# Optimization experiments

Measured on AMD Instinct MI355X. Metric: run time of the kernel, lower is better.

The kernel has to match this reference:

```python
import jax, jax.numpy as jnp
import numpy as np

N, E, DIN, H = 10000, 80000, 1024, 512
NEG = 0.2  # PyG GATv2Conv default negative_slope


def gatv2(x, src, dst, wl, bl, wr, br, att, b, n):
    # GATv2: e_ij = att . leaky_relu(Wl x_j + Wr x_i); segment softmax over dst; sum alpha * Wl x_j
    xl = x @ wl + bl            # [N, H] source transform
    xr = x @ wr + br            # [N, H] target transform
    z = jax.nn.leaky_relu(xl[src] + xr[dst], NEG)   # [E, H]
    e = z @ att                                      # [E]
    m = jax.ops.segment_max(e, dst, num_segments=n)  # per-target max (self-loops guarantee nonempty)
    p = jnp.exp(e - m[dst])
    s = jax.ops.segment_sum(p, dst, num_segments=n)
    alpha = p / (s[dst] + 1e-16)                     # [E]
    out = jax.ops.segment_sum(alpha[:, None] * xl[src], dst, num_segments=n)
    return out + b


def setup_inputs() -> dict:
    key = jax.random.key(0)
    ks = iter(jax.random.split(key, 64))
    d = {}
    d["x"] = jax.random.normal(next(ks), (N, DIN), jnp.float32)
    d["edge_index"] = jax.random.randint(next(ks), (2, E), 0, N, dtype=jnp.int32).astype(jnp.int64)
    dims = [DIN, H, H, H]
    for i in range(4):
        din = dims[i]
        sc = 1.0 / np.sqrt(din)
        d[f"wl{i+1}"] = jax.random.normal(next(ks), (din, H), jnp.float32) * sc
        d[f"bl{i+1}"] = jnp.zeros((H,), jnp.float32)
        d[f"wr{i+1}"] = jax.random.normal(next(ks), (din, H), jnp.float32) * sc
        d[f"br{i+1}"] = jnp.zeros((H,), jnp.float32)
        d[f"att{i+1}"] = jax.random.normal(next(ks), (H,), jnp.float32) * (1.0 / np.sqrt(H))
        d[f"b{i+1}"] = jnp.zeros((H,), jnp.float32)
    for name, din, dout in [("1", H, 512), ("2", 512, 256), ("3", 256, 2)]:
        d[f"lw{name}"] = jax.random.normal(next(ks), (din, dout), jnp.float32) * (1.0 / np.sqrt(din))
        d[f"lb{name}"] = jnp.zeros((dout,), jnp.float32)
    return d


def reference(x, edge_index, wl1, bl1, wr1, br1, att1, b1,
              wl2, bl2, wr2, br2, att2, b2,
              wl3, bl3, wr3, br3, att3, b3,
              wl4, bl4, wr4, br4, att4, b4,
              lw1, lb1, lw2, lb2, lw3, lb3):
    n = x.shape[0]
    loops = jnp.arange(n, dtype=edge_index.dtype)
    src = jnp.concatenate([edge_index[0], loops])  # add self-loops (PyG default)
    dst = jnp.concatenate([edge_index[1], loops])
    h = jax.nn.relu(gatv2(x, src, dst, wl1, bl1, wr1, br1, att1, b1, n))
    h = jax.nn.relu(gatv2(h, src, dst, wl2, bl2, wr2, br2, att2, b2, n))
    h = jax.nn.relu(gatv2(h, src, dst, wl3, bl3, wr3, br3, att3, b3, n))
    h = jax.nn.relu(gatv2(h, src, dst, wl4, bl4, wr4, br4, att4, b4, n))
    # dropout is identity at inference
    h = jax.nn.relu(h @ lw1 + lb1)
    h = jax.nn.relu(h @ lw2 + lb2)
    logits = h @ lw3 + lb3
    return logits, jax.nn.softmax(logits, axis=1)
```

## Files before the change

### kernel.cpp

```cpp
#include <hip/hip_runtime.h>
#include <cstdint>

#define NN 10000
#define NE 80000
#define DIN_ 1024
#define HH 512

typedef __attribute__((ext_vector_type(8))) short bf16x8;
typedef __attribute__((ext_vector_type(4))) float f32x4;
typedef unsigned short u16;
typedef unsigned int u32;

static __device__ __forceinline__ float b2f(u16 u) {
  u32 i = ((u32)u) << 16;
  return __builtin_bit_cast(float, i);
}
static __device__ __forceinline__ u16 f2b(float f) {
  u32 i = __builtin_bit_cast(u32, f);
  u32 r = (i + 0x7fffu + ((i >> 16) & 1u)) >> 16;
  return (u16)r;
}
static __device__ __forceinline__ void unpack8(uint4 u, float* f) {
  f[0] = __builtin_bit_cast(float, u.x << 16);
  f[1] = __builtin_bit_cast(float, u.x & 0xffff0000u);
  f[2] = __builtin_bit_cast(float, u.y << 16);
  f[3] = __builtin_bit_cast(float, u.y & 0xffff0000u);
  f[4] = __builtin_bit_cast(float, u.z << 16);
  f[5] = __builtin_bit_cast(float, u.z & 0xffff0000u);
  f[6] = __builtin_bit_cast(float, u.w << 16);
  f[7] = __builtin_bit_cast(float, u.w & 0xffff0000u);
}
static __device__ __forceinline__ void load8(const u16* p, float* f) { unpack8(*(const uint4*)p, f); }

#define ASYNC_CP16(gp, lp)                                                        \
  __builtin_amdgcn_global_load_lds((__attribute__((address_space(1))) void*)(gp), \
                                   (__attribute__((address_space(3))) void*)(lp), \
                                   16, 0, 0)

static __device__ __forceinline__ int float_flag(const u16* xw) {
  __shared__ int c;
  if (threadIdx.x == 0) c = 0;
  __syncthreads();
  int bad = 0;
  for (int i = threadIdx.x; i < 2048; i += blockDim.x) {
    u32 e = (xw[i] >> 7) & 0xFFu;
    if (e >= 140u) bad++;
  }
  if (bad) atomicAdd(&c, bad);
  __syncthreads();
  return c > 64;
}
static __device__ __forceinline__ int int64_flag(const u32* ew) {
  __shared__ int c;
  if (threadIdx.x == 0) c = 0;
  __syncthreads();
  int z = 0;
  for (int i = threadIdx.x; i < 256; i += blockDim.x)
    if (ew[2 * i + 1] == 0u) z++;
  if (z) atomicAdd(&c, z);
  __syncthreads();
  return c > 200;
}

__global__ void k_edges(const void* ei, int* esrc, int* edst, int* counts) {
  int f64 = int64_flag((const u32*)ei);
  int i = blockIdx.x * 256 + threadIdx.x;
  if (i < NE) {
    int sv, dv;
    if (f64) {
      sv = (int)((const long long*)ei)[i];
      dv = (int)((const long long*)ei)[NE + i];
    } else {
      sv = ((const int*)ei)[i];
      dv = ((const int*)ei)[NE + i];
    }
    esrc[i] = sv;
    edst[i] = dv;
    atomicAdd(&counts[dv], 1);
  } else if (i < NE + NN) {
    atomicAdd(&counts[i - NE], 1);
  }
}

__global__ __launch_bounds__(512) void k_scan(const int* counts, int* rowptr, int* cursor, int n) {
  __shared__ int lds[512];
  const int PER = 20;
  int t = threadIdx.x;
  int base = t * PER;
  int v[PER];
  int sum = 0;
#pragma unroll
  for (int i = 0; i < PER; i++) {
    int idx = base + i;
    v[i] = (idx < n) ? counts[idx] : 0;
    sum += v[i];
  }
  lds[t] = sum;
  __syncthreads();
  for (int off = 1; off < 512; off <<= 1) {
    int x = (t >= off) ? lds[t - off] : 0;
    __syncthreads();
    lds[t] += x;
    __syncthreads();
  }
  int run = (t > 0) ? lds[t - 1] : 0;
#pragma unroll
  for (int i = 0; i < PER; i++) {
    int idx = base + i;
    if (idx < n) {
      cursor[idx] = run;
      run += v[i];
      rowptr[idx + 1] = run;
    }
  }
  if (t == 0) rowptr[0] = 0;
}

#define SBLK 352
#define XBLK 2048
struct Prep {
  const int* esrc;
  const int* edst;
  int* cursor;
  int* col;
  const void* xin;
  u16* xout;
  const void* vin[20];
  u16* vout[20];
  int vn[20];
  const void* tin[10];
  u16* tout[10];
  int tK[10], tN[10], toff[10];
};
__global__ void k_prep(Prep a) {
  __shared__ u16 tt[32][33];
  int b = blockIdx.x;
  if (b < SBLK) {
    int i = b * 256 + threadIdx.x;
    if (i < NE) {
      int p = atomicAdd(&a.cursor[a.edst[i]], 1);
      a.col[p] = a.esrc[i];
    } else if (i < NE + NN) {
      int v = i - NE;
      int p = atomicAdd(&a.cursor[v], 1);
      a.col[p] = v;
    }
    return;
  }
  b -= SBLK;
  int f = float_flag((const u16*)a.xin);
  if (b < XBLK) {
    const int total = NN * DIN_ / 8;
    for (int g = b * 256 + threadIdx.x; g < total; g += XBLK * 256) {
      u16 o[8];
      if (f) {
        const float* p = (const float*)a.xin + (size_t)g * 8;
#pragma unroll
        for (int i = 0; i < 8; i++) o[i] = f2b(p[i]);
      } else {
        *(uint4*)o = *((const uint4*)a.xin + g);
      }
      *((uint4*)a.xout + g) = *(const uint4*)o;
    }
  } else if (b < XBLK + 20) {
    int v = b - XBLK;
    const void* in = a.vin[v];
    u16* out = a.vout[v];
    int n = a.vn[v];
    for (int i = threadIdx.x; i < n; i += 256)
      out[i] = f ? f2b(((const float*)in)[i]) : ((const u16*)in)[i];
  } else {
    int tb = b - XBLK - 20;
    int seg = 0;
#pragma unroll
    for (int i = 1; i < 10; i++)
      if (tb >= a.toff[i]) seg = i;
    int tl = tb - a.toff[seg];
    int K = a.tK[seg], N = a.tN[seg];
    int tiles_n = N >> 5;
    int n0 = (tl % tiles_n) << 5, k0 = (tl / tiles_n) << 5;
    const void* in = a.tin[seg];
    u16* out = a.tout[seg];
    int tx = threadIdx.x & 31, ty = threadIdx.x >> 5;
    for (int r = ty; r < 32; r += 8) {
      size_t idx = (size_t)(k0 + r) * N + n0 + tx;
      tt[r][tx] = f ? f2b(((const float*)in)[idx]) : ((const u16*)in)[idx];
    }
    __syncthreads();
    for (int r = ty; r < 32; r += 8) out[(size_t)(n0 + r) * K + k0 + tx] = tt[tx][r];
  }
}

__global__ __launch_bounds__(256) void k_gemm64(const u16* __restrict__ A, int lda,
                                                const u16* __restrict__ Bt,
                                                const u16* __restrict__ bias,
                                                u16* __restrict__ C,
                                                int M, int N, int K, int act,
                                                int tiles_m, int ln_tiles_n) {
  __shared__ u16 sA[2 * 64 * 32];
  __shared__ u16 sB[2 * 128 * 32];
  int id = blockIdx.x;
  int xcd = id & 7;
  int rest = id >> 3;
  int xt = rest & ((1 << ln_tiles_n) - 1);
  int yt = ((rest >> ln_tiles_n) << 3) + xcd;
  if (yt >= tiles_m) return;
  int m0 = yt << 6, n0 = xt << 7;
  int t = threadIdx.x;
  int wave = t >> 6, lane = t & 63;

  int srow = t >> 2;
  int sk = ((t & 3) ^ ((t >> 3) & 3)) * 8;
  const u16* agp[2];
  u16* la[2];
#pragma unroll
  for (int h = 0; h < 2; h++) {
    int ra = m0 + srow;
    ra = ra < M ? ra : M - 1;
    agp[h] = A + (size_t)ra * lda + h * 32 + sk;
    la[h] = sA + h * 2048 + t * 8;
  }
  const u16* bgp[4];
  u16* lb[4];
#pragma unroll
  for (int q = 0; q < 4; q++) {
    int h = q >> 1;
    int row = ((q & 1) << 6) + srow;
    bgp[q] = Bt + (size_t)(n0 + row) * K + h * 32 + sk;
    lb[q] = sB + h * 4096 + (((q & 1) << 8) + t) * 8;
  }

  int wn = wave << 5;
  int lr = lane & 15;
  int kcs = (((lane >> 4) ^ ((lr >> 1) & 3))) * 8;

  f32x4 acc[4][2];
#pragma unroll
  for (int i = 0; i < 4; i++)
#pragma unroll
    for (int j = 0; j < 2; j++) acc[i][j] = (f32x4){0.f, 0.f, 0.f, 0.f};

  for (int k0 = 0; k0 < K; k0 += 64) {
#pragma unroll
    for (int h = 0; h < 2; h++) ASYNC_CP16(agp[h] + k0, la[h]);
#pragma unroll
    for (int q = 0; q < 4; q++) ASYNC_CP16(bgp[q] + k0, lb[q]);
    __syncthreads();
    bf16x8 a[2][4], b[2][2];
#pragma unroll
    for (int s = 0; s < 2; s++) {
#pragma unroll
      for (int i = 0; i < 4; i++) a[s][i] = *(const bf16x8*)(sA + s * 2048 + (i * 16 + lr) * 32 + kcs);
#pragma unroll
      for (int j = 0; j < 2; j++) b[s][j] = *(const bf16x8*)(sB + s * 4096 + (wn + j * 16 + lr) * 32 + kcs);
    }
#pragma unroll
    for (int s = 0; s < 2; s++)
#pragma unroll
      for (int i = 0; i < 4; i++)
#pragma unroll
        for (int j = 0; j < 2; j++)
          acc[i][j] = __builtin_amdgcn_mfma_f32_16x16x32_bf16(a[s][i], b[s][j], acc[i][j], 0, 0, 0);
    __syncthreads();
  }

  int rbase = (lane >> 4) << 2;
#pragma unroll
  for (int j = 0; j < 2; j++) {
    int colc = n0 + wn + j * 16 + lr;
    float bv = b2f(bias[colc]);
#pragma unroll
    for (int i = 0; i < 4; i++) {
#pragma unroll
      for (int r = 0; r < 4; r++) {
        int row = m0 + i * 16 + rbase + r;
        if (row < M) {
          float v = acc[i][j][r] + bv;
          if (act) v = fmaxf(v, 0.f);
          C[(size_t)row * N + colc] = f2b(v);
        }
      }
    }
  }
}

__global__ __launch_bounds__(256) void k_attn5(u16* __restrict__ xlr,
                                               const u16* __restrict__ att, const u16* __restrict__ bias,
                                               const int* __restrict__ rowptr, const int* __restrict__ col,
                                               int n) {
  int node = (blockIdx.x * 256 + threadIdx.x) >> 6;
  if (node >= n) return;
  int lane = threadIdx.x & 63;
  int h0 = lane * 8;
  float a[8], r[8];
  load8(att + h0, a);
  load8(xlr + (size_t)node * 1024 + 512 + h0, r);
  int e0 = rowptr[node], e1 = rowptr[node + 1];

  float m = -3e38f, s = 0.f;
  float acc[8] = {0.f, 0.f, 0.f, 0.f, 0.f, 0.f, 0.f, 0.f};
  int j0 = col[e0];
  int j1 = col[(e0 + 1 < e1) ? e0 + 1 : e0];
  uint4 raw0 = *(const uint4*)(xlr + (size_t)j0 * 1024 + h0);
  uint4 raw1 = *(const uint4*)(xlr + (size_t)j1 * 1024 + h0);

  for (int e = e0; e < e1; e += 2) {
    bool has2 = (e + 1 < e1);
    int jn0 = col[(e + 2 < e1) ? e + 2 : e1 - 1];
    int jn1 = col[(e + 3 < e1) ? e + 3 : e1 - 1];
    uint4 p0 = *(const uint4*)(xlr + (size_t)jn0 * 1024 + h0);
    uint4 p1 = *(const uint4*)(xlr + (size_t)jn1 * 1024 + h0);
    float x0[8], x1[8];
    unpack8(raw0, x0);
    unpack8(raw1, x1);
    float pa = 0.f, pb = 0.f;
#pragma unroll
    for (int i = 0; i < 8; i++) {
      float z0 = x0[i] + r[i];
      z0 = z0 > 0.f ? z0 : 0.2f * z0;
      pa = fmaf(a[i], z0, pa);
      float z1 = x1[i] + r[i];
      z1 = z1 > 0.f ? z1 : 0.2f * z1;
      pb = fmaf(a[i], z1, pb);
    }
#pragma unroll
    for (int off = 32; off >= 1; off >>= 1) {
      pa += __shfl_xor(pa, off);
      pb += __shfl_xor(pb, off);
    }
    if (pa > m) {
      float al = __expf(m - pa);
      s = fmaf(s, al, 1.f);
#pragma unroll
      for (int i = 0; i < 8; i++) acc[i] = fmaf(acc[i], al, x0[i]);
      m = pa;
    } else {
      float w = __expf(pa - m);
      s += w;
#pragma unroll
      for (int i = 0; i < 8; i++) acc[i] = fmaf(w, x0[i], acc[i]);
    }
    if (has2) {
      if (pb > m) {
        float al = __expf(m - pb);
        s = fmaf(s, al, 1.f);
#pragma unroll
        for (int i = 0; i < 8; i++) acc[i] = fmaf(acc[i], al, x1[i]);
        m = pb;
      } else {
        float w = __expf(pb - m);
        s += w;
#pragma unroll
        for (int i = 0; i < 8; i++) acc[i] = fmaf(w, x1[i], acc[i]);
      }
    }
    raw0 = p0;
    raw1 = p1;
  }
  float inv = 1.f / (s + 1e-16f);

  float bv[8];
  load8(bias + h0, bv);
  uint4 o;
  u32 p8[8];
#pragma unroll
  for (int i = 0; i < 8; i++) {
    float v = fmaf(acc[i], inv, bv[i]);
    v = fmaxf(v, 0.f);
    p8[i] = f2b(v);
  }
  o.x = p8[0] | (p8[1] << 16);
  o.y = p8[2] | (p8[3] << 16);
  o.z = p8[4] | (p8[5] << 16);
  o.w = p8[6] | (p8[7] << 16);
  *(uint4*)(xlr + (size_t)node * 1024 + 512 + h0) = o;
}

__global__ __launch_bounds__(256) void k_head(const u16* __restrict__ h2, const u16* __restrict__ lw3,
                                              const u16* __restrict__ lb3, float* __restrict__ out, int n) {
  int row = (blockIdx.x * 256 + threadIdx.x) >> 6;
  if (row >= n) return;
  int lane = threadIdx.x & 63;
  int k0 = lane * 4;
  uint2 hu = *(const uint2*)(h2 + (size_t)row * 256 + k0);
  float hx[4];
  hx[0] = __builtin_bit_cast(float, hu.x << 16);
  hx[1] = __builtin_bit_cast(float, hu.x & 0xffff0000u);
  hx[2] = __builtin_bit_cast(float, hu.y << 16);
  hx[3] = __builtin_bit_cast(float, hu.y & 0xffff0000u);
  float wv[8];
  load8(lw3 + (size_t)k0 * 2, wv);
  float p0 = 0.f, p1 = 0.f;
#pragma unroll
  for (int i = 0; i < 4; i++) {
    p0 = fmaf(hx[i], wv[2 * i], p0);
    p1 = fmaf(hx[i], wv[2 * i + 1], p1);
  }
#pragma unroll
  for (int off = 32; off >= 1; off >>= 1) {
    p0 += __shfl_xor(p0, off);
    p1 += __shfl_xor(p1, off);
  }
  if (lane == 0) {
    float l0 = p0 + b2f(lb3[0]);
    float l1 = p1 + b2f(lb3[1]);
    float mx = fmaxf(l0, l1);
    float q0 = __expf(l0 - mx), q1 = __expf(l1 - mx);
    float si = 1.f / (q0 + q1);
    out[row * 2 + 0] = l0;
    out[row * 2 + 1] = l1;
    out[2 * n + row * 2 + 0] = q0 * si;
    out[2 * n + row * 2 + 1] = q1 * si;
  }
}

extern "C" void kernel_launch(void* const* d_in, const int* in_sizes, int n_in,
                              void* d_out, int out_size, void* d_ws, size_t ws_size,
                              hipStream_t stream) {
  (void)in_sizes; (void)n_in; (void)out_size; (void)ws_size;
  const void* x_raw = d_in[0];
  const void* ei_raw = d_in[1];
  const void *wl[4], *bl[4], *wr[4], *br[4], *att[4], *bg[4];
  for (int i = 0; i < 4; i++) {
    wl[i] = d_in[2 + i * 6 + 0];
    bl[i] = d_in[2 + i * 6 + 1];
    wr[i] = d_in[2 + i * 6 + 2];
    br[i] = d_in[2 + i * 6 + 3];
    att[i] = d_in[2 + i * 6 + 4];
    bg[i] = d_in[2 + i * 6 + 5];
  }
  const void* lw1 = d_in[26];
  const void* lb1 = d_in[27];
  const void* lw2 = d_in[28];
  const void* lb2 = d_in[29];
  const void* lw3 = d_in[30];
  const void* lb3 = d_in[31];

  size_t off = 0;
  auto alloc = [&](size_t bytes) -> void* {
    off = (off + 255) & ~(size_t)255;
    void* p = (char*)d_ws + off;
    off += bytes;
    return p;
  };
  int* esrc = (int*)alloc(NE * 4);
  int* edst = (int*)alloc(NE * 4);
  int* counts = (int*)alloc(NN * 4);
  int* rowptr = (int*)alloc((NN + 1) * 4);
  int* cursor = (int*)alloc(NN * 4);
  int* col = (int*)alloc((NE + NN) * 4);
  u16* cb = (u16*)alloc(4 * 1024 * 2);
  u16* attv = (u16*)alloc(4 * 512 * 2);
  u16* bgv = (u16*)alloc(4 * 512 * 2);
  u16* lb1v = (u16*)alloc(512 * 2);
  u16* lb2v = (u16*)alloc(256 * 2);
  u16* lw3v = (u16*)alloc(512 * 2);
  u16* lb3v = (u16*)alloc(2 * 2);
  u16* comb0 = (u16*)alloc((size_t)1024 * 1024 * 2);
  u16* combL[4];
  combL[0] = comb0;
  for (int l = 1; l < 4; l++) combL[l] = (u16*)alloc((size_t)1024 * 512 * 2);
  u16* lw1T = (u16*)alloc((size_t)512 * 512 * 2);
  u16* lw2T = (u16*)alloc((size_t)256 * 512 * 2);
  u16* xc = (u16*)alloc((size_t)NN * DIN_ * 2);
  u16* X0 = (u16*)alloc((size_t)NN * 1024 * 2);
  u16* X1 = (u16*)alloc((size_t)NN * 1024 * 2);
  u16* mlp1 = xc;
  u16* mlp2 = xc + (size_t)NN * 512;

  hipMemsetAsync(counts, 0, NN * 4, stream);
  int ET = NE + NN;
  k_edges<<<(ET + 255) / 256, 256, 0, stream>>>(ei_raw, esrc, edst, counts);
  k_scan<<<1, 512, 0, stream>>>(counts, rowptr, cursor, NN);

  Prep pa;
  pa.esrc = esrc;
  pa.edst = edst;
  pa.cursor = cursor;
  pa.col = col;
  pa.xin = x_raw;
  pa.xout = xc;
  for (int l = 0; l < 4; l++) {
    pa.vin[l * 4 + 0] = bl[l];  pa.vout[l * 4 + 0] = cb + l * 1024;        pa.vn[l * 4 + 0] = 512;
    pa.vin[l * 4 + 1] = br[l];  pa.vout[l * 4 + 1] = cb + l * 1024 + 512;  pa.vn[l * 4 + 1] = 512;
    pa.vin[l * 4 + 2] = att[l]; pa.vout[l * 4 + 2] = attv + l * 512;       pa.vn[l * 4 + 2] = 512;
    pa.vin[l * 4 + 3] = bg[l];  pa.vout[l * 4 + 3] = bgv + l * 512;        pa.vn[l * 4 + 3] = 512;
  }
  pa.vin[16] = lb1; pa.vout[16] = lb1v; pa.vn[16] = 512;
  pa.vin[17] = lb2; pa.vout[17] = lb2v; pa.vn[17] = 256;
  pa.vin[18] = lw3; pa.vout[18] = lw3v; pa.vn[18] = 512;
  pa.vin[19] = lb3; pa.vout[19] = lb3v; pa.vn[19] = 2;
  const void* tin[10] = {wl[0], wr[0], wl[1], wr[1], wl[2], wr[2], wl[3], wr[3], lw1, lw2};
  u16* tout[10] = {comb0, comb0 + (size_t)512 * 1024,
                   combL[1], combL[1] + (size_t)512 * 512,
                   combL[2], combL[2] + (size_t)512 * 512,
                   combL[3], combL[3] + (size_t)512 * 512,
                   lw1T, lw2T};
  int tK[10] = {1024, 1024, 512, 512, 512, 512, 512, 512, 512, 512};
  int tN[10] = {512, 512, 512, 512, 512, 512, 512, 512, 512, 256};
  int acc_off = 0;
  for (int i = 0; i < 10; i++) {
    pa.tin[i] = tin[i];
    pa.tout[i] = tout[i];
    pa.tK[i] = tK[i];
    pa.tN[i] = tN[i];
    pa.toff[i] = acc_off;
    acc_off += (tN[i] >> 5) * (tK[i] >> 5);
  }
  k_prep<<<SBLK + XBLK + 20 + acc_off, 256, 0, stream>>>(pa);

  auto gemm = [&](const u16* A, int lda, const u16* Bt, const u16* bias, u16* C,
                  int M, int Nn, int K, int act) {
    int tiles_m = (M + 63) >> 6;
    int tiles_n = Nn >> 7;
    int ln = (tiles_n == 8) ? 3 : (tiles_n == 4) ? 2 : 1;
    int mgrp = (tiles_m + 7) >> 3;
    int blocks = (mgrp << 3) * tiles_n;
    k_gemm64<<<blocks, 256, 0, stream>>>(A, lda, Bt, bias, C, M, Nn, K, act, tiles_m, ln);
  };
  auto attn = [&](u16* xlr, int l) {
    k_attn5<<<(NN * 64 + 255) / 256, 256, 0, stream>>>(xlr, attv + l * 512, bgv + l * 512,
                                                       rowptr, col, NN);
  };

  gemm(xc, 1024, comb0, cb + 0 * 1024, X0, NN, 1024, 1024, 0);
  attn(X0, 0);
  gemm(X0 + 512, 1024, combL[1], cb + 1 * 1024, X1, NN, 1024, 512, 0);
  attn(X1, 1);
  gemm(X1 + 512, 1024, combL[2], cb + 2 * 1024, X0, NN, 1024, 512, 0);
  attn(X0, 2);
  gemm(X0 + 512, 1024, combL[3], cb + 3 * 1024, X1, NN, 1024, 512, 0);
  attn(X1, 3);

  gemm(X1 + 512, 1024, lw1T, lb1v, mlp1, NN, 512, 512, 1);
  gemm(mlp1, 512, lw2T, lb2v, mlp2, NN, 256, 512, 1);
  k_head<<<(NN * 64 + 255) / 256, 256, 0, stream>>>(mlp2, lw3v, lb3v, (float*)d_out, NN);
}
```

Measured before the change: 368.1 us.

## Double-buffer GEMM K-loop with async copies and fold x conversion into scan

The GEMM main loop now uses two 32-wide K stages in shared memory. The next tile's async copies are issued before computing the current one, and explicit vmcnt waits with raw barriers replace the two syncthreads per 64-wide step. This is meant to hide global-load latency behind MFMA work. Separately, the fp32-to-bf16 conversion of x moves out of the prep kernel into the single-block scan launch, so the conversion blocks run alongside the scan instead of padding the prep grid. The raw barrier and waitcnt scheduling adds hazard risk if the compiler reorders LDS accesses.

```diff
diff --git a/kernel.cpp b/kernel.cpp
--- a/kernel.cpp
+++ b/kernel.cpp
@@ -82,49 +82,65 @@
   }
 }
 
-__global__ __launch_bounds__(512) void k_scan(const int* counts, int* rowptr, int* cursor, int n) {
-  __shared__ int lds[512];
-  const int PER = 20;
-  int t = threadIdx.x;
-  int base = t * PER;
-  int v[PER];
-  int sum = 0;
-#pragma unroll
-  for (int i = 0; i < PER; i++) {
-    int idx = base + i;
-    v[i] = (idx < n) ? counts[idx] : 0;
-    sum += v[i];
-  }
-  lds[t] = sum;
-  __syncthreads();
-  for (int off = 1; off < 512; off <<= 1) {
-    int x = (t >= off) ? lds[t - off] : 0;
+#define CONVB 2047
+__global__ __launch_bounds__(512) void k_scanconv(const int* counts, int* rowptr, int* cursor, int n,
+                                                  const void* xin, u16* xout) {
+  if (blockIdx.x == 0) {
+    __shared__ int lds[512];
+    const int PER = 20;
+    int t = threadIdx.x;
+    int base = t * PER;
+    int v[PER];
+    int sum = 0;
+#pragma unroll
+    for (int i = 0; i < PER; i++) {
+      int idx = base + i;
+      v[i] = (idx < n) ? counts[idx] : 0;
+      sum += v[i];
+    }
+    lds[t] = sum;
     __syncthreads();
-    lds[t] += x;
-    __syncthreads();
-  }
-  int run = (t > 0) ? lds[t - 1] : 0;
-#pragma unroll
-  for (int i = 0; i < PER; i++) {
-    int idx = base + i;
-    if (idx < n) {
-      cursor[idx] = run;
-      run += v[i];
-      rowptr[idx + 1] = run;
-    }
-  }
-  if (t == 0) rowptr[0] = 0;
+    for (int off = 1; off < 512; off <<= 1) {
+      int x = (t >= off) ? lds[t - off] : 0;
+      __syncthreads();
+      lds[t] += x;
+      __syncthreads();
+    }
+    int run = (t > 0) ? lds[t - 1] : 0;
+#pragma unroll
+    for (int i = 0; i < PER; i++) {
+      int idx = base + i;
+      if (idx < n) {
+        cursor[idx] = run;
+        run += v[i];
+        rowptr[idx + 1] = run;
+      }
+    }
+    if (t == 0) rowptr[0] = 0;
+    return;
+  }
+  int f = float_flag((const u16*)xin);
+  const int total = NN * DIN_ / 8;
+  for (int g = (blockIdx.x - 1) * 512 + threadIdx.x; g < total; g += CONVB * 512) {
+    u16 o[8];
+    if (f) {
+      const float* p = (const float*)xin + (size_t)g * 8;
+#pragma unroll
+      for (int i = 0; i < 8; i++) o[i] = f2b(p[i]);
+    } else {
+      *(uint4*)o = *((const uint4*)xin + g);
+    }
+    *((uint4*)xout + g) = *(const uint4*)o;
+  }
 }
 
 #define SBLK 352
-#define XBLK 2048
 struct Prep {
   const int* esrc;
   const int* edst;
   int* cursor;
   int* col;
   const void* xin;
-  u16* xout;
   const void* vin[20];
   u16* vout[20];
   int vn[20];
@@ -149,28 +165,15 @@
   }
   b -= SBLK;
   int f = float_flag((const u16*)a.xin);
-  if (b < XBLK) {
-    const int total = NN * DIN_ / 8;
-    for (int g = b * 256 + threadIdx.x; g < total; g += XBLK * 256) {
-      u16 o[8];
-      if (f) {
-        const float* p = (const float*)a.xin + (size_t)g * 8;
-#pragma unroll
-        for (int i = 0; i < 8; i++) o[i] = f2b(p[i]);
-      } else {
-        *(uint4*)o = *((const uint4*)a.xin + g);
-      }
-      *((uint4*)a.xout + g) = *(const uint4*)o;
-    }
-  } else if (b < XBLK + 20) {
-    int v = b - XBLK;
+  if (b < 20) {
+    int v = b;
     const void* in = a.vin[v];
     u16* out = a.vout[v];
     int n = a.vn[v];
     for (int i = threadIdx.x; i < n; i += 256)
       out[i] = f ? f2b(((const float*)in)[i]) : ((const u16*)in)[i];
   } else {
-    int tb = b - XBLK - 20;
+    int tb = b - 20;
     int seg = 0;
 #pragma unroll
     for (int i = 1; i < 10; i++)
@@ -197,8 +200,7 @@
                                                 u16* __restrict__ C,
                                                 int M, int N, int K, int act,
                                                 int tiles_m, int ln_tiles_n) {
-  __shared__ u16 sA[2 * 64 * 32];
-  __shared__ u16 sB[2 * 128 * 32];
+  __shared__ u16 smem[12288];
   int id = blockIdx.x;
   int xcd = id & 7;
   int rest = id >> 3;
@@ -211,24 +213,14 @@
 
   int srow = t >> 2;
   int sk = ((t & 3) ^ ((t >> 3) & 3)) * 8;
-  const u16* agp[2];
-  u16* la[2];
-#pragma unroll
-  for (int h = 0; h < 2; h++) {
-    int ra = m0 + srow;
-    ra = ra < M ? ra : M - 1;
-    agp[h] = A + (size_t)ra * lda + h * 32 + sk;
-    la[h] = sA + h * 2048 + t * 8;
-  }
-  const u16* bgp[4];
-  u16* lb[4];
-#pragma unroll
-  for (int q = 0; q < 4; q++) {
-    int h = q >> 1;
-    int row = ((q & 1) << 6) + srow;
-    bgp[q] = Bt + (size_t)(n0 + row) * K + h * 32 + sk;
-    lb[q] = sB + h * 4096 + (((q & 1) << 8) + t) * 8;
-  }
+  int ra = m0 + srow;
+  ra = ra < M ? ra : M - 1;
+  const u16* ag = A + (size_t)ra * lda + sk;
+  const u16* bg0 = Bt + (size_t)(n0 + srow) * K + sk;
+  const u16* bg1 = Bt + (size_t)(n0 + 64 + srow) * K + sk;
+  int lA = t * 8;
+  int lB0 = 2048 + t * 8;
+  int lB1 = 2048 + (256 + t) * 8;
 
   int wn = wave << 5;
   int lr = lane & 15;
@@ -240,28 +232,36 @@
 #pragma unroll
     for (int j = 0; j < 2; j++) acc[i][j] = (f32x4){0.f, 0.f, 0.f, 0.f};
 
-  for (int k0 = 0; k0 < K; k0 += 64) {
-#pragma unroll
-    for (int h = 0; h < 2; h++) ASYNC_CP16(agp[h] + k0, la[h]);
-#pragma unroll
-    for (int q = 0; q < 4; q++) ASYNC_CP16(bgp[q] + k0, lb[q]);
-    __syncthreads();
-    bf16x8 a[2][4], b[2][2];
-#pragma unroll
-    for (int s = 0; s < 2; s++) {
-#pragma unroll
-      for (int i = 0; i < 4; i++) a[s][i] = *(const bf16x8*)(sA + s * 2048 + (i * 16 + lr) * 32 + kcs);
-#pragma unroll
-      for (int j = 0; j < 2; j++) b[s][j] = *(const bf16x8*)(sB + s * 4096 + (wn + j * 16 + lr) * 32 + kcs);
-    }
-#pragma unroll
-    for (int s = 0; s < 2; s++)
-#pragma unroll
-      for (int i = 0; i < 4; i++)
-#pragma unroll
-        for (int j = 0; j < 2; j++)
-          acc[i][j] = __builtin_amdgcn_mfma_f32_16x16x32_bf16(a[s][i], b[s][j], acc[i][j], 0, 0, 0);
-    __syncthreads();
+  ASYNC_CP16(ag, smem + lA);
+  ASYNC_CP16(bg0, smem + lB0);
+  ASYNC_CP16(bg1, smem + lB1);
+
+  int NT = K >> 5;
+  for (int it = 0; it < NT; ++it) {
+    int cb = (it & 1) * 6144;
+    int nb = 6144 - cb;
+    if (it + 1 < NT) {
+      int ko = (it + 1) << 5;
+      ASYNC_CP16(ag + ko, smem + nb + lA);
+      ASYNC_CP16(bg0 + ko, smem + nb + lB0);
+      ASYNC_CP16(bg1 + ko, smem + nb + lB1);
+      asm volatile("s_waitcnt vmcnt(3)" ::: "memory");
+    } else {
+      asm volatile("s_waitcnt vmcnt(0)" ::: "memory");
+    }
+    __builtin_amdgcn_s_barrier();
+    __builtin_amdgcn_sched_barrier(0);
+    bf16x8 a[4], b[2];
+#pragma unroll
+    for (int i = 0; i < 4; i++) a[i] = *(const bf16x8*)(smem + cb + (i * 16 + lr) * 32 + kcs);
+#pragma unroll
+    for (int j = 0; j < 2; j++) b[j] = *(const bf16x8*)(smem + cb + 2048 + (wn + j * 16 + lr) * 32 + kcs);
+#pragma unroll
+    for (int i = 0; i < 4; i++)
+#pragma unroll
+      for (int j = 0; j < 2; j++)
+        acc[i][j] = __builtin_amdgcn_mfma_f32_16x16x32_bf16(a[i], b[j], acc[i][j], 0, 0, 0);
+    __builtin_amdgcn_s_barrier();
   }
 
   int rbase = (lane >> 4) << 2;
@@ -471,7 +471,7 @@
   hipMemsetAsync(counts, 0, NN * 4, stream);
   int ET = NE + NN;
   k_edges<<<(ET + 255) / 256, 256, 0, stream>>>(ei_raw, esrc, edst, counts);
-  k_scan<<<1, 512, 0, stream>>>(counts, rowptr, cursor, NN);
+  k_scanconv<<<1 + CONVB, 512, 0, stream>>>(counts, rowptr, cursor, NN, x_raw, xc);
 
   Prep pa;
   pa.esrc = esrc;
@@ -479,7 +479,6 @@
   pa.cursor = cursor;
   pa.col = col;
   pa.xin = x_raw;
-  pa.xout = xc;
   for (int l = 0; l < 4; l++) {
     pa.vin[l * 4 + 0] = bl[l];  pa.vout[l * 4 + 0] = cb + l * 1024;        pa.vn[l * 4 + 0] = 512;
     pa.vin[l * 4 + 1] = br[l];  pa.vout[l * 4 + 1] = cb + l * 1024 + 512;  pa.vn[l * 4 + 1] = 512;
@@ -507,7 +506,7 @@
     pa.toff[i] = acc_off;
     acc_off += (tN[i] >> 5) * (tK[i] >> 5);
   }
-  k_prep<<<SBLK + XBLK + 20 + acc_off, 256, 0, stream>>>(pa);
+  k_prep<<<SBLK + 20 + acc_off, 256, 0, stream>>>(pa);
 
   auto gemm = [&](const u16* A, int lda, const u16* Bt, const u16* bias, u16* C,
                   int M, int Nn, int K, int act) {
```

Measured after the change: 378.6 us. +2.8%, slower.

## Fuse MLP head into one kernel and move x conversion into scan kernel

Applied to the files above, without the earlier changes.

Replaces the two MLP GEMM launches and the head kernel with a single fused kernel. Each 64-row tile computes layer1, layer2 and the 2-way head, keeping the intermediates in LDS instead of global memory. Separately, the bf16 conversion of x moves from the prep kernel into the single-block scan launch, so it runs alongside the scan instead of the scatter. The fused MLP uses a large LDS footprint (~136KB) with few blocks (157), so occupancy and parallelism are limited.

```diff
diff --git a/kernel.cpp b/kernel.cpp
--- a/kernel.cpp
+++ b/kernel.cpp
@@ -82,49 +82,65 @@
   }
 }
 
-__global__ __launch_bounds__(512) void k_scan(const int* counts, int* rowptr, int* cursor, int n) {
-  __shared__ int lds[512];
-  const int PER = 20;
-  int t = threadIdx.x;
-  int base = t * PER;
-  int v[PER];
-  int sum = 0;
-#pragma unroll
-  for (int i = 0; i < PER; i++) {
-    int idx = base + i;
-    v[i] = (idx < n) ? counts[idx] : 0;
-    sum += v[i];
-  }
-  lds[t] = sum;
-  __syncthreads();
-  for (int off = 1; off < 512; off <<= 1) {
-    int x = (t >= off) ? lds[t - off] : 0;
+#define CONVB 2047
+__global__ __launch_bounds__(512) void k_scanconv(const int* counts, int* rowptr, int* cursor, int n,
+                                                  const void* xin, u16* xout) {
+  if (blockIdx.x == 0) {
+    __shared__ int lds[512];
+    const int PER = 20;
+    int t = threadIdx.x;
+    int base = t * PER;
+    int v[PER];
+    int sum = 0;
+#pragma unroll
+    for (int i = 0; i < PER; i++) {
+      int idx = base + i;
+      v[i] = (idx < n) ? counts[idx] : 0;
+      sum += v[i];
+    }
+    lds[t] = sum;
     __syncthreads();
-    lds[t] += x;
-    __syncthreads();
-  }
-  int run = (t > 0) ? lds[t - 1] : 0;
-#pragma unroll
-  for (int i = 0; i < PER; i++) {
-    int idx = base + i;
-    if (idx < n) {
-      cursor[idx] = run;
-      run += v[i];
-      rowptr[idx + 1] = run;
-    }
-  }
-  if (t == 0) rowptr[0] = 0;
+    for (int off = 1; off < 512; off <<= 1) {
+      int x = (t >= off) ? lds[t - off] : 0;
+      __syncthreads();
+      lds[t] += x;
+      __syncthreads();
+    }
+    int run = (t > 0) ? lds[t - 1] : 0;
+#pragma unroll
+    for (int i = 0; i < PER; i++) {
+      int idx = base + i;
+      if (idx < n) {
+        cursor[idx] = run;
+        run += v[i];
+        rowptr[idx + 1] = run;
+      }
+    }
+    if (t == 0) rowptr[0] = 0;
+    return;
+  }
+  int f = float_flag((const u16*)xin);
+  const int total = NN * DIN_ / 8;
+  for (int g = (blockIdx.x - 1) * 512 + threadIdx.x; g < total; g += CONVB * 512) {
+    u16 o[8];
+    if (f) {
+      const float* p = (const float*)xin + (size_t)g * 8;
+#pragma unroll
+      for (int i = 0; i < 8; i++) o[i] = f2b(p[i]);
+    } else {
+      *(uint4*)o = *((const uint4*)xin + g);
+    }
+    *((uint4*)xout + g) = *(const uint4*)o;
+  }
 }
 
 #define SBLK 352
-#define XBLK 2048
 struct Prep {
   const int* esrc;
   const int* edst;
   int* cursor;
   int* col;
   const void* xin;
-  u16* xout;
   const void* vin[20];
   u16* vout[20];
   int vn[20];
@@ -149,28 +165,15 @@
   }
   b -= SBLK;
   int f = float_flag((const u16*)a.xin);
-  if (b < XBLK) {
-    const int total = NN * DIN_ / 8;
-    for (int g = b * 256 + threadIdx.x; g < total; g += XBLK * 256) {
-      u16 o[8];
-      if (f) {
-        const float* p = (const float*)a.xin + (size_t)g * 8;
-#pragma unroll
-        for (int i = 0; i < 8; i++) o[i] = f2b(p[i]);
-      } else {
-        *(uint4*)o = *((const uint4*)a.xin + g);
-      }
-      *((uint4*)a.xout + g) = *(const uint4*)o;
-    }
-  } else if (b < XBLK + 20) {
-    int v = b - XBLK;
+  if (b < 20) {
+    int v = b;
     const void* in = a.vin[v];
     u16* out = a.vout[v];
     int n = a.vn[v];
     for (int i = threadIdx.x; i < n; i += 256)
       out[i] = f ? f2b(((const float*)in)[i]) : ((const u16*)in)[i];
   } else {
-    int tb = b - XBLK - 20;
+    int tb = b - 20;
     int seg = 0;
 #pragma unroll
     for (int i = 1; i < 10; i++)
@@ -284,6 +287,146 @@
   }
 }
 
+__global__ __launch_bounds__(256) void k_mlp(const u16* __restrict__ A, int lda,
+                                             const u16* __restrict__ w1T, const u16* __restrict__ b1,
+                                             const u16* __restrict__ w2T, const u16* __restrict__ b2,
+                                             const u16* __restrict__ w3, const u16* __restrict__ b3,
+                                             float* __restrict__ out, int M) {
+  __shared__ u16 smem[18432 + 33280 + 16896];
+  u16* stg = smem;
+  u16* h1 = smem + 18432;
+  u16* h2 = smem + 18432 + 33280;
+  int m0 = blockIdx.x * 64;
+  int t = threadIdx.x;
+  int wave = t >> 6, lane = t & 63;
+  int lr = lane & 15;
+  int kcs = (((lane >> 4) ^ ((lr >> 1) & 3))) * 8;
+  int kdir = (lane >> 4) * 8;
+  int srow = t >> 2;
+  int sk = ((t & 3) ^ ((t >> 3) & 3)) * 8;
+  int rbase = (lane >> 4) << 2;
+
+  int ra = m0 + srow;
+  ra = ra < M ? ra : M - 1;
+  const u16* ag = A + (size_t)ra * lda + sk;
+
+  {
+    f32x4 acc[4][8];
+#pragma unroll
+    for (int i = 0; i < 4; i++)
+#pragma unroll
+      for (int j = 0; j < 8; j++) acc[i][j] = (f32x4){0.f, 0.f, 0.f, 0.f};
+    for (int k0 = 0; k0 < 512; k0 += 32) {
+#pragma unroll
+      for (int q = 0; q < 8; q++)
+        ASYNC_CP16(w1T + (size_t)(q * 64 + srow) * 512 + k0 + sk, stg + (q * 256 + t) * 8);
+      ASYNC_CP16(ag + k0, stg + 16384 + t * 8);
+      __syncthreads();
+      bf16x8 a[4], b[8];
+#pragma unroll
+      for (int i = 0; i < 4; i++) a[i] = *(const bf16x8*)(stg + 16384 + (i * 16 + lr) * 32 + kcs);
+#pragma unroll
+      for (int j = 0; j < 8; j++) b[j] = *(const bf16x8*)(stg + (wave * 128 + j * 16 + lr) * 32 + kcs);
+#pragma unroll
+      for (int i = 0; i < 4; i++)
+#pragma unroll
+        for (int j = 0; j < 8; j++)
+          acc[i][j] = __builtin_amdgcn_mfma_f32_16x16x32_bf16(a[i], b[j], acc[i][j], 0, 0, 0);
+      __syncthreads();
+    }
+#pragma unroll
+    for (int j = 0; j < 8; j++) {
+      int col = wave * 128 + j * 16 + lr;
+      float bv = b2f(b1[col]);
+#pragma unroll
+      for (int i = 0; i < 4; i++)
+#pragma unroll
+        for (int r = 0; r < 4; r++) {
+          int row = i * 16 + rbase + r;
+          float v = acc[i][j][r] + bv;
+          h1[row * 520 + col] = f2b(fmaxf(v, 0.f));
+        }
+    }
+  }
+  __syncthreads();
+
+  {
+    f32x4 acc[4][4];
+#pragma unroll
+    for (int i = 0; i < 4; i++)
+#pragma unroll
+      for (int j = 0; j < 4; j++) acc[i][j] = (f32x4){0.f, 0.f, 0.f, 0.f};
+    for (int k0 = 0; k0 < 512; k0 += 32) {
+#pragma unroll
+      for (int q = 0; q < 4; q++)
+        ASYNC_CP16(w2T + (size_t)(q * 64 + srow) * 512 + k0 + sk, stg + (q * 256 + t) * 8);
+      __syncthreads();
+      bf16x8 a[4], b[4];
+#pragma unroll
+      for (int i = 0; i < 4; i++) a[i] = *(const bf16x8*)(h1 + (i * 16 + lr) * 520 + k0 + kdir);
+#pragma unroll
+      for (int j = 0; j < 4; j++) b[j] = *(const bf16x8*)(stg + (wave * 64 + j * 16 + lr) * 32 + kcs);
+#pragma unroll
+      for (int i = 0; i < 4; i++)
+#pragma unroll
+        for (int j = 0; j < 4; j++)
+          acc[i][j] = __builtin_amdgcn_mfma_f32_16x16x32_bf16(a[i], b[j], acc[i][j], 0, 0, 0);
+      __syncthreads();
+    }
+#pragma unroll
+    for (int j = 0; j < 4; j++) {
+      int col = wave * 64 + j * 16 + lr;
+      float bv = b2f(b2[col]);
+#pragma unroll
+      for (int i = 0; i < 4; i++)
+#pragma unroll
+        for (int r = 0; r < 4; r++) {
+          int row = i * 16 + rbase + r;
+          float v = acc[i][j][r] + bv;
+          h2[row * 264 + col] = f2b(fmaxf(v, 0.f));
+        }
+    }
+  }
+  __syncthreads();
+
+  float wv[8];
+  load8(w3 + (size_t)(lane * 4) * 2, wv);
+  float bl0 = b2f(b3[0]), bl1 = b2f(b3[1]);
+  for (int rr = 0; rr < 16; rr++) {
+    int row = wave * 16 + rr;
+    int grow = m0 + row;
+    if (grow >= M) break;
+    uint2 hu = *(const uint2*)(h2 + row * 264 + lane * 4);
+    float hx[4];
+    hx[0] = __builtin_bit_cast(float, hu.x << 16);
+    hx[1] = __builtin_bit_cast(float, hu.x & 0xffff0000u);
+    hx[2] = __builtin_bit_cast(float, hu.y << 16);
+    hx[3] = __builtin_bit_cast(float, hu.y & 0xffff0000u);
+    float p0 = 0.f, p1 = 0.f;
+#pragma unroll
+    for (int i = 0; i < 4; i++) {
+      p0 = fmaf(hx[i], wv[2 * i], p0);
+      p1 = fmaf(hx[i], wv[2 * i + 1], p1);
+    }
+#pragma unroll
+    for (int off = 32; off >= 1; off >>= 1) {
+      p0 += __shfl_xor(p0, off);
+      p1 += __shfl_xor(p1, off);
+    }
+    if (lane == 0) {
+      float l0 = p0 + bl0;
+      float l1 = p1 + bl1;
+      float mx = fmaxf(l0, l1);
+      float q0 = __expf(l0 - mx), q1 = __expf(l1 - mx);
+      float si = 1.f / (q0 + q1);
+      out[grow * 2 + 0] = l0;
+      out[grow * 2 + 1] = l1;
+      out[2 * M + grow * 2 + 0] = q0 * si;
+      out[2 * M + grow * 2 + 1] = q1 * si;
+    }
+  }
+}
+
 __global__ __launch_bounds__(256) void k_attn5(u16* __restrict__ xlr,
                                                const u16* __restrict__ att, const u16* __restrict__ bias,
                                                const int* __restrict__ rowptr, const int* __restrict__ col,
@@ -374,44 +517,6 @@
   o.z = p8[4] | (p8[5] << 16);
   o.w = p8[6] | (p8[7] << 16);
   *(uint4*)(xlr + (size_t)node * 1024 + 512 + h0) = o;
-}
-
-__global__ __launch_bounds__(256) void k_head(const u16* __restrict__ h2, const u16* __restrict__ lw3,
-                                              const u16* __restrict__ lb3, float* __restrict__ out, int n) {
-  int row = (blockIdx.x * 256 + threadIdx.x) >> 6;
-  if (row >= n) return;
-  int lane = threadIdx.x & 63;
-  int k0 = lane * 4;
-  uint2 hu = *(const uint2*)(h2 + (size_t)row * 256 + k0);
-  float hx[4];
-  hx[0] = __builtin_bit_cast(float, hu.x << 16);
-  hx[1] = __builtin_bit_cast(float, hu.x & 0xffff0000u);
-  hx[2] = __builtin_bit_cast(float, hu.y << 16);
-  hx[3] = __builtin_bit_cast(float, hu.y & 0xffff0000u);
-  float wv[8];
-  load8(lw3 + (size_t)k0 * 2, wv);
-  float p0 = 0.f, p1 = 0.f;
-#pragma unroll
-  for (int i = 0; i < 4; i++) {
-    p0 = fmaf(hx[i], wv[2 * i], p0);
-    p1 = fmaf(hx[i], wv[2 * i + 1], p1);
-  }
-#pragma unroll
-  for (int off = 32; off >= 1; off >>= 1) {
-    p0 += __shfl_xor(p0, off);
-    p1 += __shfl_xor(p1, off);
-  }
-  if (lane == 0) {
-    float l0 = p0 + b2f(lb3[0]);
-    float l1 = p1 + b2f(lb3[1]);
-    float mx = fmaxf(l0, l1);
-    float q0 = __expf(l0 - mx), q1 = __expf(l1 - mx);
-    float si = 1.f / (q0 + q1);
-    out[row * 2 + 0] = l0;
-    out[row * 2 + 1] = l1;
-    out[2 * n + row * 2 + 0] = q0 * si;
-    out[2 * n + row * 2 + 1] = q1 * si;
-  }
 }
 
 extern "C" void kernel_launch(void* const* d_in, const int* in_sizes, int n_in,
@@ -465,13 +570,11 @@
   u16* xc = (u16*)alloc((size_t)NN * DIN_ * 2);
   u16* X0 = (u16*)alloc((size_t)NN * 1024 * 2);
   u16* X1 = (u16*)alloc((size_t)NN * 1024 * 2);
-  u16* mlp1 = xc;
-  u16* mlp2 = xc + (size_t)NN * 512;
 
   hipMemsetAsync(counts, 0, NN * 4, stream);
   int ET = NE + NN;
   k_edges<<<(ET + 255) / 256, 256, 0, stream>>>(ei_raw, esrc, edst, counts);
-  k_scan<<<1, 512, 0, stream>>>(counts, rowptr, cursor, NN);
+  k_scanconv<<<1 + CONVB, 512, 0, stream>>>(counts, rowptr, cursor, NN, x_raw, xc);
 
   Prep pa;
   pa.esrc = esrc;
@@ -479,7 +582,6 @@
   pa.cursor = cursor;
   pa.col = col;
   pa.xin = x_raw;
-  pa.xout = xc;
   for (int l = 0; l < 4; l++) {
     pa.vin[l * 4 + 0] = bl[l];  pa.vout[l * 4 + 0] = cb + l * 1024;        pa.vn[l * 4 + 0] = 512;
     pa.vin[l * 4 + 1] = br[l];  pa.vout[l * 4 + 1] = cb + l * 1024 + 512;  pa.vn[l * 4 + 1] = 512;
@@ -507,7 +609,7 @@
     pa.toff[i] = acc_off;
     acc_off += (tN[i] >> 5) * (tK[i] >> 5);
   }
-  k_prep<<<SBLK + XBLK + 20 + acc_off, 256, 0, stream>>>(pa);
+  k_prep<<<SBLK + 20 + acc_off, 256, 0, stream>>>(pa);
 
   auto gemm = [&](const u16* A, int lda, const u16* Bt, const u16* bias, u16* C,
                   int M, int Nn, int K, int act) {
@@ -532,7 +634,6 @@
   gemm(X0 + 512, 1024, combL[3], cb + 3 * 1024, X1, NN, 1024, 512, 0);
   attn(X1, 3);
 
-  gemm(X1 + 512, 1024, lw1T, lb1v, mlp1, NN, 512, 512, 1);
-  gemm(mlp1, 512, lw2T, lb2v, mlp2, NN, 256, 512, 1);
-  k_head<<<(NN * 64 + 255) / 256, 256, 0, stream>>>(mlp2, lw3v, lb3v, (float*)d_out, NN);
-}
+  k_mlp<<<(NN + 63) / 64, 256, 0, stream>>>(X1 + 512, 1024, lw1T, lb1v, lw2T, lb2v,
+                                            lw3v, lb3v, (float*)d_out, NN);
+}
```

Measured after the change: 372.2 us. Within noise of the previous version (+1.1%).
